# Optimization experiments

Measured on AMD Instinct MI355X. Metric: run time of the kernel, lower is better.

## Reference

```python
import jax, jax.numpy as jnp
import numpy as np

N = 100000      # nodes
E = 1600000     # edges
FX = 128        # raw node feature dim
MAXZ = 100      # z embedding / one-hot size
HID = 128       # hidden_channels
NL = 3          # num_layers
G = 512         # num graphs
BN_EPS = 1e-5


def _lin(key, din, dout):
    return jax.random.normal(key, (din, dout), jnp.float32) * (1.0 / np.sqrt(din))


def setup_inputs() -> dict:
    key = jax.random.key(0)
    ks = jax.random.split(key, 64)
    d = {}
    d["x"] = jax.random.normal(ks[0], (N, FX), jnp.float32)
    d["z"] = jax.random.randint(ks[1], (N,), 0, MAXZ)
    d["edge_index"] = jax.random.randint(ks[2], (2, E), 0, N)
    d["batch"] = jnp.sort(jax.random.randint(ks[3], (N,), 0, G))
    in0 = FX + 2 * MAXZ  # z_emb concatenated twice (faithful to source)
    ki = 4
    for l in range(NL):
        din = in0 if l == 0 else HID
        d[f"W1_{l}"] = _lin(ks[ki], din, HID); ki += 1
        d[f"b1_{l}"] = jnp.zeros((HID,), jnp.float32)
        d[f"W2_{l}"] = _lin(ks[ki], HID, HID); ki += 1
        d[f"b2_{l}"] = jnp.zeros((HID,), jnp.float32)
        d[f"g_{l}"] = jnp.ones((HID,), jnp.float32)
        d[f"be_{l}"] = jnp.zeros((HID,), jnp.float32)
    d["Wl1"] = _lin(ks[ki], NL * HID, HID); ki += 1
    d["bl1"] = jnp.zeros((HID,), jnp.float32)
    d["Wl2"] = _lin(ks[ki], HID, 1); ki += 1
    d["bl2"] = jnp.zeros((1,), jnp.float32)
    return d


def _gin_layer(h, src, dst, W1, b1, W2, b2, g, be):
    # GINConv with eps=0: nn(x + sum_{j->i} x_j)
    agg = jax.ops.segment_sum(h[src], dst, num_segments=N)  # [N, d]
    m = h + agg
    m = jax.nn.relu(m @ W1 + b1)
    m = jax.nn.relu(m @ W2 + b2)
    # training-mode BatchNorm1d over node axis (biased variance)
    mu = m.mean(0)
    var = jnp.mean((m - mu) ** 2, axis=0)
    return (m - mu) * jax.lax.rsqrt(var + BN_EPS) * g + be


def reference(x, z, edge_index, batch,
              W1_0, b1_0, W2_0, b2_0, g_0, be_0,
              W1_1, b1_1, W2_1, b2_1, g_1, be_1,
              W1_2, b1_2, W2_2, b2_2, g_2, be_2,
              Wl1, bl1, Wl2, bl2):
    src, dst = edge_index[0], edge_index[1]
    z_emb = jax.nn.one_hot(z, MAXZ, dtype=jnp.float32)  # [N, MAXZ]
    h = jnp.concatenate([z_emb, x], axis=1)
    h = jnp.concatenate([z_emb, h], axis=1)  # faithful double concat -> [N, FX+2*MAXZ]
    params = [(W1_0, b1_0, W2_0, b2_0, g_0, be_0),
              (W1_1, b1_1, W2_1, b2_1, g_1, be_1),
              (W1_2, b1_2, W2_2, b2_2, g_2, be_2)]
    xs = []
    for p in params:
        h = _gin_layer(h, src, dst, *p)
        xs.append(h)
    hcat = jnp.concatenate(xs, axis=1)  # jumping knowledge: [N, NL*HID]
    # global_mean_pool over graph ids
    counts = jax.ops.segment_sum(jnp.ones((N,), jnp.float32), batch, num_segments=G)
    pooled = jax.ops.segment_sum(hcat, batch, num_segments=G) / jnp.maximum(counts, 1.0)[:, None]
    out = jax.nn.relu(pooled @ Wl1 + bl1)
    # dropout is identity in eval / reference mode
    out = out @ Wl2 + bl2  # [G, 1]
    return out
```

## Files before the change

kernel.cpp:

```cpp
#include <hip/hip_runtime.h>
#include <hip/hip_bf16.h>

#define NN 100000
#define NROWS_PAD 100032
#define EE 1600000
#define GG 512
#define NPB 256
#define NB  ((NN + NPB - 1) / NPB)
#define PCHUNK 4096
#define PBLOCKS ((EE + PCHUNK - 1) / PCHUNK)
#define SBANK 8
static constexpr float BN_EPS = 1e-5f;

typedef _Float16 half8 __attribute__((ext_vector_type(8)));
typedef float floatx4 __attribute__((ext_vector_type(4)));


__global__ __launch_bounds__(256) void k_bhist(const int* __restrict__ EI,
                                               int* __restrict__ bcount)
{
    __shared__ int h[NB];
    const int t = threadIdx.x;
    for (int i = t; i < NB; i += 256) h[i] = 0;
    __syncthreads();
    const int e0 = blockIdx.x * PCHUNK;
    const int e1 = (e0 + PCHUNK < EE) ? e0 + PCHUNK : EE;
    for (int e = e0 + t; e < e1; e += 256)
        atomicAdd(&h[EI[EE + e] >> 8], 1);
    __syncthreads();
    for (int i = t; i < NB; i += 256)
        if (h[i]) atomicAdd(&bcount[i], h[i]);
}

__global__ __launch_bounds__(512) void k_bscan(const int* __restrict__ bcount,
                                               int* __restrict__ bstart,
                                               int* __restrict__ bcursor,
                                               int* __restrict__ row_start)
{
    __shared__ int s[512];
    int t = threadIdx.x;
    int v = (t < NB) ? bcount[t] : 0;
    s[t] = v;
    __syncthreads();
    for (int off = 1; off < 512; off <<= 1) {
        int u = (t >= off) ? s[t - off] : 0;
        __syncthreads();
        s[t] += u;
        __syncthreads();
    }
    if (t < NB) { int ex = s[t] - v; bstart[t] = ex; bcursor[t] = ex; }
    if (t == 0) { bstart[NB] = EE; row_start[NN] = EE; }
}

__global__ __launch_bounds__(256) void k_part(const int* __restrict__ EI,
                                              int* __restrict__ bcursor,
                                              int* __restrict__ ebuf)
{
    __shared__ int h[NB];
    __shared__ int cur[NB];
    const int t = threadIdx.x;
    for (int i = t; i < NB; i += 256) h[i] = 0;
    __syncthreads();
    const int e0 = blockIdx.x * PCHUNK;
    const int e1 = (e0 + PCHUNK < EE) ? e0 + PCHUNK : EE;
    for (int e = e0 + t; e < e1; e += 256)
        atomicAdd(&h[EI[EE + e] >> 8], 1);
    __syncthreads();
    for (int i = t; i < NB; i += 256)
        cur[i] = h[i] ? atomicAdd(&bcursor[i], h[i]) : 0;
    __syncthreads();
    for (int e = e0 + t; e < e1; e += 256) {
        int s = EI[e], d = EI[EE + e];
        int pos = atomicAdd(&cur[d >> 8], 1);
        ebuf[pos] = s | ((d & (NPB - 1)) << 17);
    }
}

__global__ __launch_bounds__(256) void k_csrbucket(const int* __restrict__ ebuf,
                                                   const int* __restrict__ bstart,
                                                   int* __restrict__ row_start,
                                                   int* __restrict__ ssrc)
{
    __shared__ int cnt[NPB];
    __shared__ int cur[NPB];
    const int b = blockIdx.x, t = threadIdx.x;
    cnt[t] = 0;
    __syncthreads();
    const int e0 = bstart[b], e1 = bstart[b + 1];
    for (int e = e0 + t; e < e1; e += 256) {
        unsigned p = (unsigned)__builtin_nontemporal_load(&ebuf[e]);
        atomicAdd(&cnt[p >> 17], 1);
    }
    __syncthreads();
    int myc = cnt[t];
    for (int off = 1; off < 256; off <<= 1) {
        int u = (t >= off) ? cnt[t - off] : 0;
        __syncthreads();
        cnt[t] += u;
        __syncthreads();
    }
    int pos0 = e0 + cnt[t] - myc;
    int idx = b * NPB + t;
    if (idx < NN) row_start[idx] = pos0;
    cur[t] = pos0;
    __syncthreads();
    for (int e = e0 + t; e < e1; e += 256) {
        unsigned p = (unsigned)__builtin_nontemporal_load(&ebuf[e]);
        int pos = atomicAdd(&cur[p >> 17], 1);
        ssrc[pos] = (int)(p & 0x1FFFFu);
    }
}


__global__ __launch_bounds__(256) void k_xcast(const float* __restrict__ X,
                                               _Float16* __restrict__ Xh)
{
    int idx = blockIdx.x * 256 + threadIdx.x;
    const float4* src = (const float4*)X;
    float4 a = src[idx * 2], b = src[idx * 2 + 1];
    half8 o = { (_Float16)a.x, (_Float16)a.y, (_Float16)a.z, (_Float16)a.w,
                (_Float16)b.x, (_Float16)b.y, (_Float16)b.z, (_Float16)b.w };
    *(half8*)&Xh[idx * 8] = o;
}

__device__ __forceinline__ void bn_sc_sh(const float* statsL,
                                         const float* g, const float* be, int k,
                                         float& sc, float& sh)
{
    float cs = 0.f, cq = 0.f;
    #pragma unroll
    for (int b = 0; b < SBANK; ++b) {
        cs += statsL[b * 256 + k];
        cq += statsL[b * 256 + 128 + k];
    }
    float inv_n = 1.0f / (float)NN;
    float mu = cs * inv_n;
    float var = cq * inv_n - mu * mu;
    sc = g[k] * rsqrtf(var + BN_EPS);
    sh = be[k] - mu * sc;
}

__global__ __launch_bounds__(256) void k_prep(
    const float* __restrict__ W1, const float* __restrict__ W2,
    const float* __restrict__ statsPrev,
    const float* __restrict__ g, const float* __restrict__ be,
    _Float16* __restrict__ Wt1, _Float16* __restrict__ Wt2,
    float* __restrict__ cvec, int l)
{
    int b = blockIdx.x, t = threadIdx.x;
    if (b < 64) {
        int idx = b * 256 + t;
        int n = idx >> 7, k = idx & 127;
        if (l == 0) {
            Wt1[idx] = (_Float16)W1[(200 + k) * 128 + n];
        } else {
            float sc, sh;
            bn_sc_sh(statsPrev, g, be, k, sc, sh);
            Wt1[idx] = (_Float16)(sc * W1[k * 128 + n]);
        }
    } else if (b < 128) {
        int idx = (b - 64) * 256 + t;
        int n = idx >> 7, k = idx & 127;
        Wt2[idx] = (_Float16)W2[k * 128 + n];
    } else if (t < 128) {
        float acc = 0.f;
        if (l != 0) {
            for (int k = 0; k < 128; ++k) {
                float sc, sh;
                bn_sc_sh(statsPrev, g, be, k, sc, sh);
                acc = fmaf(sh, W1[k * 128 + t], acc);
            }
        }
        cvec[t] = acc;
    }
}


#define MM_CORE_G(Ah, Wth)                                                   \
    const int lane = tid & 63;                                               \
    const int wv = tid >> 6;                                                 \
    const int ml = lane & 15;                                                \
    const int quad = lane >> 4;                                              \
    const int wr = wv >> 1, wc = wv & 1;                                     \
    floatx4 acc[2][4];                                                       \
    for (int r = 0; r < 2; ++r)                                              \
        for (int t = 0; t < 4; ++t)                                          \
            acc[r][t] = (floatx4){0.f, 0.f, 0.f, 0.f};                       \
    {                                                                        \
        const size_t ar0 = (size_t)(row0 + 32 * wr + ml) * 128;              \
        const size_t ar1 = ar0 + (size_t)16 * 128;                           \
        _Pragma("unroll")                                                    \
        for (int kq = 0; kq < 4; ++kq) {                                     \
            int k0 = kq * 32;                                                \
            half8 a0 = *(const half8*)&Ah[ar0 + k0 + quad * 8];              \
            half8 a1 = *(const half8*)&Ah[ar1 + k0 + quad * 8];              \
            _Pragma("unroll")                                                \
            for (int t = 0; t < 4; ++t) {                                    \
                half8 bf = *(const half8*)&Wth[(size_t)(64 * wc + 16 * t + ml) * 128 + k0 + quad * 8]; \
                acc[0][t] = __builtin_amdgcn_mfma_f32_16x16x32_f16(a0, bf, acc[0][t], 0, 0, 0); \
                acc[1][t] = __builtin_amdgcn_mfma_f32_16x16x32_f16(a1, bf, acc[1][t], 0, 0, 0); \
            }                                                                \
        }                                                                    \
    }

__global__ __launch_bounds__(256) void k_mm_embed(
    const _Float16* __restrict__ Ah, const _Float16* __restrict__ Wth,
    const int* __restrict__ Z, const float* __restrict__ W1,
    _Float16* __restrict__ Ph)
{
    const int tid = threadIdx.x;
    const int row0 = blockIdx.x * 64;
    MM_CORE_G(Ah, Wth)
    #pragma unroll
    for (int r = 0; r < 2; ++r)
        #pragma unroll
        for (int j = 0; j < 4; ++j) {
            int grow = row0 + 32 * wr + 16 * r + quad * 4 + j;
            if (grow < NN) {
                int zv = Z[grow];
                const float* w0 = &W1[zv * 128];
                const float* w1 = &W1[(100 + zv) * 128];
                #pragma unroll
                for (int t = 0; t < 4; ++t) {
                    int gcol = 64 * wc + 16 * t + ml;
                    float v = acc[r][t][j] + w0[gcol] + w1[gcol];
                    Ph[(size_t)grow * 128 + gcol] = (_Float16)v;
                }
            }
        }
}

__global__ __launch_bounds__(256) void k_mm1(
    const _Float16* __restrict__ Ah, const _Float16* __restrict__ Wth,
    _Float16* __restrict__ Ph)
{
    const int tid = threadIdx.x;
    const int row0 = blockIdx.x * 64;
    MM_CORE_G(Ah, Wth)
    #pragma unroll
    for (int r = 0; r < 2; ++r)
        #pragma unroll
        for (int j = 0; j < 4; ++j) {
            int grow = row0 + 32 * wr + 16 * r + quad * 4 + j;
            if (grow < NN) {
                #pragma unroll
                for (int t = 0; t < 4; ++t) {
                    int gcol = 64 * wc + 16 * t + ml;
                    Ph[(size_t)grow * 128 + gcol] = (_Float16)acc[r][t][j];
                }
            }
        }
}

__global__ __launch_bounds__(256) void k_mm2(
    const _Float16* __restrict__ Ah, const _Float16* __restrict__ Wth,
    const float* __restrict__ b2, _Float16* __restrict__ Oh,
    float* __restrict__ statsL)
{
    __shared__ float cs[128];
    __shared__ float cq[128];
    const int tid = threadIdx.x;
    const int row0 = blockIdx.x * 64;
    if (tid < 128) { cs[tid] = 0.f; cq[tid] = 0.f; }
    __syncthreads();

    MM_CORE_G(Ah, Wth)

    float b2v[4];
    #pragma unroll
    for (int t = 0; t < 4; ++t) b2v[t] = b2[64 * wc + 16 * t + ml];
    float st[4] = {0.f, 0.f, 0.f, 0.f};
    float qt[4] = {0.f, 0.f, 0.f, 0.f};
    #pragma unroll
    for (int r = 0; r < 2; ++r)
        #pragma unroll
        for (int j = 0; j < 4; ++j) {
            int grow = row0 + 32 * wr + 16 * r + quad * 4 + j;
            if (grow < NN) {
                #pragma unroll
                for (int t = 0; t < 4; ++t) {
                    int gcol = 64 * wc + 16 * t + ml;
                    float v = fmaxf(acc[r][t][j] + b2v[t], 0.f);
                    Oh[(size_t)grow * 128 + gcol] = (_Float16)v;
                    st[t] += v;
                    qt[t] += v * v;
                }
            }
        }
    #pragma unroll
    for (int t = 0; t < 4; ++t) {
        int gcol = 64 * wc + 16 * t + ml;
        atomicAdd(&cs[gcol], st[t]);
        atomicAdd(&cq[gcol], qt[t]);
    }
    __syncthreads();
    if (tid < 128) {
        float* bank = statsL + (blockIdx.x & (SBANK - 1)) * 256;
        atomicAdd(&bank[tid], cs[tid]);
        atomicAdd(&bank[128 + tid], cq[tid]);
    }
}


__global__ __launch_bounds__(256) void k_aggregate(
    const _Float16* __restrict__ Ph, const int* __restrict__ row_start,
    const int* __restrict__ ssrc, const float* __restrict__ b1,
    const float* __restrict__ cvec, _Float16* __restrict__ Mh)
{
    int idx = blockIdx.x * 256 + threadIdx.x;
    int node = idx >> 4, q = idx & 15;
    if (node >= NN) return;
    int s0 = row_start[node], s1 = row_start[node + 1];
    float degp1 = (float)(s1 - s0 + 1);
    float acc[8];
    half8 pv = *(const half8*)&Ph[(size_t)node * 128 + q * 8];
    #pragma unroll
    for (int j = 0; j < 8; ++j)
        acc[j] = (float)pv[j] + fmaf(degp1, cvec[q * 8 + j], b1[q * 8 + j]);
    int e = s0;
    for (; e + 7 < s1; e += 8) {
        int sidx[8];
        #pragma unroll
        for (int u = 0; u < 8; ++u)
            sidx[u] = __builtin_nontemporal_load(&ssrc[e + u]);
        half8 v[8];
        #pragma unroll
        for (int u = 0; u < 8; ++u)
            v[u] = *(const half8*)&Ph[(size_t)sidx[u] * 128 + q * 8];
        #pragma unroll
        for (int j = 0; j < 8; ++j)
            acc[j] += (((float)v[0][j] + (float)v[1][j]) + ((float)v[2][j] + (float)v[3][j]))
                    + (((float)v[4][j] + (float)v[5][j]) + ((float)v[6][j] + (float)v[7][j]));
    }
    for (; e + 1 < s1; e += 2) {
        int sa = __builtin_nontemporal_load(&ssrc[e]);
        int sb = __builtin_nontemporal_load(&ssrc[e + 1]);
        half8 va = *(const half8*)&Ph[(size_t)sa * 128 + q * 8];
        half8 vb = *(const half8*)&Ph[(size_t)sb * 128 + q * 8];
        #pragma unroll
        for (int j = 0; j < 8; ++j) acc[j] += (float)va[j] + (float)vb[j];
    }
    if (e < s1) {
        int sa = __builtin_nontemporal_load(&ssrc[e]);
        half8 va = *(const half8*)&Ph[(size_t)sa * 128 + q * 8];
        #pragma unroll
        for (int j = 0; j < 8; ++j) acc[j] += (float)va[j];
    }
    half8 o;
    #pragma unroll
    for (int j = 0; j < 8; ++j) o[j] = (_Float16)fmaxf(acc[j], 0.f);
    __builtin_nontemporal_store(o, (half8*)&Mh[(size_t)node * 128 + q * 8]);
}


__global__ __launch_bounds__(128) void k_pool(
    const _Float16* __restrict__ Ah, const int* __restrict__ batch,
    const float* __restrict__ statsL,
    const float* __restrict__ g_, const float* __restrict__ be,
    float* __restrict__ pooled, int loff)
{
    __shared__ float red[8][128];
    int g = blockIdx.x;
    int t = threadIdx.x;
    int rg = t >> 4, seg = t & 15;
    int lo = 0, hi = NN;
    while (lo < hi) { int mid = (lo + hi) >> 1; if (batch[mid] < g) lo = mid + 1; else hi = mid; }
    int s = lo;
    lo = s; hi = NN;
    while (lo < hi) { int mid = (lo + hi) >> 1; if (batch[mid] < g + 1) lo = mid + 1; else hi = mid; }
    int e = lo;
    float acc[8] = {};
    for (int i = s + rg; i < e; i += 8) {
        half8 v = *(const half8*)&Ah[(size_t)i * 128 + seg * 8];
        #pragma unroll
        for (int j = 0; j < 8; ++j) acc[j] += (float)v[j];
    }
    #pragma unroll
    for (int j = 0; j < 8; ++j) red[rg][seg * 8 + j] = acc[j];
    __syncthreads();
    int cnt = e - s;
    float inv = 1.0f / (float)(cnt > 0 ? cnt : 1);
    if (t < 128) {
        float s_ = 0.f;
        #pragma unroll
        for (int r = 0; r < 8; ++r) s_ += red[r][t];
        float sc, sh;
        bn_sc_sh(statsL, g_, be, t, sc, sh);
        pooled[g * 384 + loff + t] = fmaf(sc, s_ * inv, sh);
    }
}

__global__ __launch_bounds__(128) void k_final(
    const float* __restrict__ pooled,
    const float* __restrict__ Wl1, const float* __restrict__ bl1,
    const float* __restrict__ Wl2, const float* __restrict__ bl2,
    float* __restrict__ out)
{
    __shared__ float pr[384];
    __shared__ float red[128];
    int g = blockIdx.x, j = threadIdx.x;
    for (int i = j; i < 384; i += 128) pr[i] = pooled[g * 384 + i];
    __syncthreads();
    float acc = bl1[j];
    for (int k = 0; k < 384; ++k) acc = fmaf(pr[k], Wl1[k * 128 + j], acc);
    float r = fmaxf(acc, 0.f) * Wl2[j];
    red[j] = r;
    __syncthreads();
    for (int off = 64; off > 0; off >>= 1) {
        if (j < off) red[j] += red[j + off];
        __syncthreads();
    }
    if (j == 0) out[g] = red[0] + bl2[0];
}

extern "C" void kernel_launch(void* const* d_in, const int* in_sizes, int n_in,
                              void* d_out, int out_size, void* d_ws, size_t ws_size,
                              hipStream_t stream)
{
    const float* x     = (const float*)d_in[0];
    const int*   z     = (const int*)d_in[1];
    const int*   ei    = (const int*)d_in[2];
    const int*   batch = (const int*)d_in[3];
    const float* W1a[3] = {(const float*)d_in[4],  (const float*)d_in[10], (const float*)d_in[16]};
    const float* b1a[3] = {(const float*)d_in[5],  (const float*)d_in[11], (const float*)d_in[17]};
    const float* W2a[3] = {(const float*)d_in[6],  (const float*)d_in[12], (const float*)d_in[18]};
    const float* b2a[3] = {(const float*)d_in[7],  (const float*)d_in[13], (const float*)d_in[19]};
    const float* ga[3]  = {(const float*)d_in[8],  (const float*)d_in[14], (const float*)d_in[20]};
    const float* bea[3] = {(const float*)d_in[9],  (const float*)d_in[15], (const float*)d_in[21]};
    const float* Wl1 = (const float*)d_in[22];
    const float* bl1 = (const float*)d_in[23];
    const float* Wl2 = (const float*)d_in[24];
    const float* bl2 = (const float*)d_in[25];
    float* out = (float*)d_out;

    char* ws = (char*)d_ws;
    size_t off = 0;
    auto alloc = [&](size_t bytes) {
        void* p = ws + off;
        off += (bytes + 255) & ~(size_t)255;
        return p;
    };
    _Float16* Xh  = (_Float16*)alloc((size_t)NROWS_PAD * 128 * 2);
    _Float16* Ph  = (_Float16*)alloc((size_t)NROWS_PAD * 128 * 2);
    _Float16* Mh  = (_Float16*)alloc((size_t)NROWS_PAD * 128 * 2);
    _Float16* Ahb = (_Float16*)alloc((size_t)NROWS_PAD * 128 * 2);
    _Float16* Wt1 = (_Float16*)alloc((size_t)128 * 128 * 2);
    _Float16* Wt2 = (_Float16*)alloc((size_t)128 * 128 * 2);
    int*   ebuf     = (int*)alloc((size_t)EE * 4);
    int*   ssrc     = (int*)alloc((size_t)EE * 4);
    int*   row_st   = (int*)alloc((size_t)(NN + 1) * 4);
    int*   bcount   = (int*)alloc((size_t)NB * 4);
    int*   bstart   = (int*)alloc((size_t)(NB + 1) * 4);
    int*   bcursor  = (int*)alloc((size_t)NB * 4);
    float* cvec     = (float*)alloc(128 * 4);
    float* stats    = (float*)alloc((size_t)3 * SBANK * 256 * 4);
    float* pooled   = (float*)alloc((size_t)GG * 384 * 4);

    const int gemmBlocks = (NN + 63) / 64;
    const int aggBlocks  = (NN * 16 + 255) / 256;

    hipMemsetAsync(stats, 0, (size_t)3 * SBANK * 256 * 4, stream);
    hipMemsetAsync(bcount, 0, (size_t)NB * 4, stream);
    k_xcast<<<(NN * 128 / 8 + 255) / 256, 256, 0, stream>>>(x, Xh);
    k_bhist<<<PBLOCKS, 256, 0, stream>>>(ei, bcount);
    k_bscan<<<1, 512, 0, stream>>>(bcount, bstart, bcursor, row_st);
    k_part<<<PBLOCKS, 256, 0, stream>>>(ei, bcursor, ebuf);
    k_csrbucket<<<NB, 256, 0, stream>>>(ebuf, bstart, row_st, ssrc);

    for (int l = 0; l < 3; ++l) {
        float* statsL   = stats + (size_t)l * SBANK * 256;
        const float* statsPrev = (l > 0) ? stats + (size_t)(l - 1) * SBANK * 256 : stats;
        const float* pg   = (l > 0) ? ga[l - 1] : ga[0];
        const float* pbe  = (l > 0) ? bea[l - 1] : bea[0];
        k_prep<<<129, 256, 0, stream>>>(W1a[l], W2a[l], statsPrev, pg, pbe,
                                        Wt1, Wt2, cvec, l);
        if (l == 0)
            k_mm_embed<<<gemmBlocks, 256, 0, stream>>>(Xh, Wt1, z, W1a[0], Ph);
        else
            k_mm1<<<gemmBlocks, 256, 0, stream>>>(Ahb, Wt1, Ph);
        k_aggregate<<<aggBlocks, 256, 0, stream>>>(Ph, row_st, ssrc, b1a[l], cvec, Mh);
        k_mm2<<<gemmBlocks, 256, 0, stream>>>(Mh, Wt2, b2a[l], Ahb, statsL);
        k_pool<<<GG, 128, 0, stream>>>(Ahb, batch, statsL, ga[l], bea[l],
                                       pooled, l * 128);
    }
    k_final<<<GG, 128, 0, stream>>>(pooled, Wl1, bl1, Wl2, bl2, out);
}
```

Before: 699.8 us.

## Sort nodes by degree to balance aggregate kernel wavefront work

Adds a degree histogram, a scan and a fill pass that build a permutation of nodes ordered by descending in-degree. The aggregate kernel then processes nodes in that order, so each wavefront handles nodes of similar degree and loop divergence is reduced. The cost is three small extra kernel launches and an extra indirection per node, and neighbouring slots now touch scattered node rows, which loses locality on Ph and Mh accesses.

```diff
diff --git a/kernel.cpp b/kernel.cpp
--- a/kernel.cpp
+++ b/kernel.cpp
@@ -10,6 +10,7 @@
 #define PCHUNK 4096
 #define PBLOCKS ((EE + PCHUNK - 1) / PCHUNK)
 #define SBANK 8
+#define DBIN 64
 static constexpr float BN_EPS = 1e-5f;
 
 typedef _Float16 half8 __attribute__((ext_vector_type(8)));
@@ -108,6 +109,46 @@
         unsigned p = (unsigned)__builtin_nontemporal_load(&ebuf[e]);
         int pos = atomicAdd(&cur[p >> 17], 1);
         ssrc[pos] = (int)(p & 0x1FFFFu);
+    }
+}
+
+
+__global__ __launch_bounds__(256) void k_dhist(const int* __restrict__ row_start,
+                                               int* __restrict__ dcount)
+{
+    __shared__ int h[DBIN];
+    const int t = threadIdx.x;
+    if (t < DBIN) h[t] = 0;
+    __syncthreads();
+    int i = blockIdx.x * 256 + t;
+    if (i < NN) {
+        int deg = row_start[i + 1] - row_start[i];
+        int bin = deg < DBIN ? deg : DBIN - 1;
+        atomicAdd(&h[bin], 1);
+    }
+    __syncthreads();
+    if (t < DBIN && h[t]) atomicAdd(&dcount[t], h[t]);
+}
+
+__global__ __launch_bounds__(64) void k_dscan(const int* __restrict__ dcount,
+                                              int* __restrict__ dcur)
+{
+    int b = threadIdx.x;
+    int off = 0;
+    for (int b2 = b + 1; b2 < DBIN; ++b2) off += dcount[b2];
+    dcur[b] = off;
+}
+
+__global__ __launch_bounds__(256) void k_dfill(const int* __restrict__ row_start,
+                                               int* __restrict__ dcur,
+                                               int* __restrict__ perm)
+{
+    int i = blockIdx.x * 256 + threadIdx.x;
+    if (i < NN) {
+        int deg = row_start[i + 1] - row_start[i];
+        int bin = deg < DBIN ? deg : DBIN - 1;
+        int pos = atomicAdd(&dcur[bin], 1);
+        perm[pos] = i;
     }
 }
 
@@ -304,12 +345,14 @@
 
 __global__ __launch_bounds__(256) void k_aggregate(
     const _Float16* __restrict__ Ph, const int* __restrict__ row_start,
-    const int* __restrict__ ssrc, const float* __restrict__ b1,
-    const float* __restrict__ cvec, _Float16* __restrict__ Mh)
+    const int* __restrict__ ssrc, const int* __restrict__ perm,
+    const float* __restrict__ b1, const float* __restrict__ cvec,
+    _Float16* __restrict__ Mh)
 {
     int idx = blockIdx.x * 256 + threadIdx.x;
-    int node = idx >> 4, q = idx & 15;
-    if (node >= NN) return;
+    int slot = idx >> 4, q = idx & 15;
+    if (slot >= NN) return;
+    int node = perm[slot];
     int s0 = row_start[node], s1 = row_start[node + 1];
     float degp1 = (float)(s1 - s0 + 1);
     float acc[8];
@@ -449,23 +492,31 @@
     int*   ebuf     = (int*)alloc((size_t)EE * 4);
     int*   ssrc     = (int*)alloc((size_t)EE * 4);
     int*   row_st   = (int*)alloc((size_t)(NN + 1) * 4);
+    int*   perm     = (int*)alloc((size_t)NN * 4);
     int*   bcount   = (int*)alloc((size_t)NB * 4);
     int*   bstart   = (int*)alloc((size_t)(NB + 1) * 4);
     int*   bcursor  = (int*)alloc((size_t)NB * 4);
+    int*   dcount   = (int*)alloc((size_t)DBIN * 4);
+    int*   dcur     = (int*)alloc((size_t)DBIN * 4);
     float* cvec     = (float*)alloc(128 * 4);
     float* stats    = (float*)alloc((size_t)3 * SBANK * 256 * 4);
     float* pooled   = (float*)alloc((size_t)GG * 384 * 4);
 
     const int gemmBlocks = (NN + 63) / 64;
     const int aggBlocks  = (NN * 16 + 255) / 256;
+    const int nodeBlocks = (NN + 255) / 256;
 
     hipMemsetAsync(stats, 0, (size_t)3 * SBANK * 256 * 4, stream);
     hipMemsetAsync(bcount, 0, (size_t)NB * 4, stream);
+    hipMemsetAsync(dcount, 0, (size_t)DBIN * 4, stream);
     k_xcast<<<(NN * 128 / 8 + 255) / 256, 256, 0, stream>>>(x, Xh);
     k_bhist<<<PBLOCKS, 256, 0, stream>>>(ei, bcount);
     k_bscan<<<1, 512, 0, stream>>>(bcount, bstart, bcursor, row_st);
     k_part<<<PBLOCKS, 256, 0, stream>>>(ei, bcursor, ebuf);
     k_csrbucket<<<NB, 256, 0, stream>>>(ebuf, bstart, row_st, ssrc);
+    k_dhist<<<nodeBlocks, 256, 0, stream>>>(row_st, dcount);
+    k_dscan<<<1, 64, 0, stream>>>(dcount, dcur);
+    k_dfill<<<nodeBlocks, 256, 0, stream>>>(row_st, dcur, perm);
 
     for (int l = 0; l < 3; ++l) {
         float* statsL   = stats + (size_t)l * SBANK * 256;
@@ -478,7 +529,8 @@
             k_mm_embed<<<gemmBlocks, 256, 0, stream>>>(Xh, Wt1, z, W1a[0], Ph);
         else
             k_mm1<<<gemmBlocks, 256, 0, stream>>>(Ahb, Wt1, Ph);
-        k_aggregate<<<aggBlocks, 256, 0, stream>>>(Ph, row_st, ssrc, b1a[l], cvec, Mh);
+        k_aggregate<<<aggBlocks, 256, 0, stream>>>(Ph, row_st, ssrc, perm,
+                                                   b1a[l], cvec, Mh);
         k_mm2<<<gemmBlocks, 256, 0, stream>>>(Mh, Wt2, b2a[l], Ahb, statsL);
         k_pool<<<GG, 128, 0, stream>>>(Ahb, batch, statsL, ga[l], bea[l],
                                        pooled, l * 128);
```

Result: slower. 978.6 us (+39.8%).

## Move BatchNorm statistics from GEMM epilogue atomics into per-graph pool reduction

Applied to the files above, without the earlier changes.

The per-column sum and sum-of-squares for BatchNorm are no longer accumulated with shared and global atomics in the mm2 epilogue. Instead, the pool kernel, which already reads every row, also accumulates squares and writes per-graph sums. A new single-block kernel reduces these over graphs into scale and shift vectors, and the final kernel applies the affine transform to the pooled means. This takes the atomics and extra syncs out of the GEMM and removes a memset, at the cost of an extra serial single-block launch per layer that loops over 512 graphs.

```diff
diff --git a/kernel.cpp b/kernel.cpp
--- a/kernel.cpp
+++ b/kernel.cpp
@@ -9,7 +9,6 @@
 #define NB  ((NN + NPB - 1) / NPB)
 #define PCHUNK 4096
 #define PBLOCKS ((EE + PCHUNK - 1) / PCHUNK)
-#define SBANK 8
 static constexpr float BN_EPS = 1e-5f;
 
 typedef _Float16 half8 __attribute__((ext_vector_type(8)));
@@ -123,27 +122,9 @@
     *(half8*)&Xh[idx * 8] = o;
 }
 
-__device__ __forceinline__ void bn_sc_sh(const float* statsL,
-                                         const float* g, const float* be, int k,
-                                         float& sc, float& sh)
-{
-    float cs = 0.f, cq = 0.f;
-    #pragma unroll
-    for (int b = 0; b < SBANK; ++b) {
-        cs += statsL[b * 256 + k];
-        cq += statsL[b * 256 + 128 + k];
-    }
-    float inv_n = 1.0f / (float)NN;
-    float mu = cs * inv_n;
-    float var = cq * inv_n - mu * mu;
-    sc = g[k] * rsqrtf(var + BN_EPS);
-    sh = be[k] - mu * sc;
-}
-
 __global__ __launch_bounds__(256) void k_prep(
     const float* __restrict__ W1, const float* __restrict__ W2,
-    const float* __restrict__ statsPrev,
-    const float* __restrict__ g, const float* __restrict__ be,
+    const float* __restrict__ scshPrev,
     _Float16* __restrict__ Wt1, _Float16* __restrict__ Wt2,
     float* __restrict__ cvec, int l)
 {
@@ -154,9 +135,7 @@
         if (l == 0) {
             Wt1[idx] = (_Float16)W1[(200 + k) * 128 + n];
         } else {
-            float sc, sh;
-            bn_sc_sh(statsPrev, g, be, k, sc, sh);
-            Wt1[idx] = (_Float16)(sc * W1[k * 128 + n]);
+            Wt1[idx] = (_Float16)(scshPrev[k] * W1[k * 128 + n]);
         }
     } else if (b < 128) {
         int idx = (b - 64) * 256 + t;
@@ -164,13 +143,9 @@
         Wt2[idx] = (_Float16)W2[k * 128 + n];
     } else if (t < 128) {
         float acc = 0.f;
-        if (l != 0) {
-            for (int k = 0; k < 128; ++k) {
-                float sc, sh;
-                bn_sc_sh(statsPrev, g, be, k, sc, sh);
-                acc = fmaf(sh, W1[k * 128 + t], acc);
-            }
-        }
+        if (l != 0)
+            for (int k = 0; k < 128; ++k)
+                acc = fmaf(scshPrev[128 + k], W1[k * 128 + t], acc);
         cvec[t] = acc;
     }
 }
@@ -254,23 +229,14 @@
 
 __global__ __launch_bounds__(256) void k_mm2(
     const _Float16* __restrict__ Ah, const _Float16* __restrict__ Wth,
-    const float* __restrict__ b2, _Float16* __restrict__ Oh,
-    float* __restrict__ statsL)
-{
-    __shared__ float cs[128];
-    __shared__ float cq[128];
+    const float* __restrict__ b2, _Float16* __restrict__ Oh)
+{
     const int tid = threadIdx.x;
     const int row0 = blockIdx.x * 64;
-    if (tid < 128) { cs[tid] = 0.f; cq[tid] = 0.f; }
-    __syncthreads();
-
     MM_CORE_G(Ah, Wth)
-
     float b2v[4];
     #pragma unroll
     for (int t = 0; t < 4; ++t) b2v[t] = b2[64 * wc + 16 * t + ml];
-    float st[4] = {0.f, 0.f, 0.f, 0.f};
-    float qt[4] = {0.f, 0.f, 0.f, 0.f};
     #pragma unroll
     for (int r = 0; r < 2; ++r)
         #pragma unroll
@@ -282,23 +248,9 @@
                     int gcol = 64 * wc + 16 * t + ml;
                     float v = fmaxf(acc[r][t][j] + b2v[t], 0.f);
                     Oh[(size_t)grow * 128 + gcol] = (_Float16)v;
-                    st[t] += v;
-                    qt[t] += v * v;
                 }
             }
         }
-    #pragma unroll
-    for (int t = 0; t < 4; ++t) {
-        int gcol = 64 * wc + 16 * t + ml;
-        atomicAdd(&cs[gcol], st[t]);
-        atomicAdd(&cq[gcol], qt[t]);
-    }
-    __syncthreads();
-    if (tid < 128) {
-        float* bank = statsL + (blockIdx.x & (SBANK - 1)) * 256;
-        atomicAdd(&bank[tid], cs[tid]);
-        atomicAdd(&bank[128 + tid], cq[tid]);
-    }
 }
 
 
@@ -355,9 +307,7 @@
 
 __global__ __launch_bounds__(128) void k_pool(
     const _Float16* __restrict__ Ah, const int* __restrict__ batch,
-    const float* __restrict__ statsL,
-    const float* __restrict__ g_, const float* __restrict__ be,
-    float* __restrict__ pooled, int loff)
+    float* __restrict__ gsum, float* __restrict__ gsq, int* __restrict__ gcnt)
 {
     __shared__ float red[8][128];
     int g = blockIdx.x;
@@ -370,28 +320,57 @@
     while (lo < hi) { int mid = (lo + hi) >> 1; if (batch[mid] < g + 1) lo = mid + 1; else hi = mid; }
     int e = lo;
     float acc[8] = {};
+    float accq[8] = {};
     for (int i = s + rg; i < e; i += 8) {
         half8 v = *(const half8*)&Ah[(size_t)i * 128 + seg * 8];
         #pragma unroll
-        for (int j = 0; j < 8; ++j) acc[j] += (float)v[j];
+        for (int j = 0; j < 8; ++j) {
+            float f = (float)v[j];
+            acc[j] += f;
+            accq[j] += f * f;
+        }
     }
     #pragma unroll
     for (int j = 0; j < 8; ++j) red[rg][seg * 8 + j] = acc[j];
     __syncthreads();
-    int cnt = e - s;
-    float inv = 1.0f / (float)(cnt > 0 ? cnt : 1);
+    float s_ = 0.f;
+    #pragma unroll
+    for (int r = 0; r < 8; ++r) s_ += red[r][t];
+    __syncthreads();
+    #pragma unroll
+    for (int j = 0; j < 8; ++j) red[rg][seg * 8 + j] = accq[j];
+    __syncthreads();
+    float q_ = 0.f;
+    #pragma unroll
+    for (int r = 0; r < 8; ++r) q_ += red[r][t];
+    gsum[(size_t)g * 128 + t] = s_;
+    gsq[(size_t)g * 128 + t] = q_;
+    if (t == 0) gcnt[g] = (e - s) > 0 ? (e - s) : 1;
+}
+
+__global__ __launch_bounds__(256) void k_statsred(
+    const float* __restrict__ gsum, const float* __restrict__ gsq,
+    const float* __restrict__ g_, const float* __restrict__ be,
+    float* __restrict__ scsh)
+{
+    int t = threadIdx.x;
     if (t < 128) {
-        float s_ = 0.f;
-        #pragma unroll
-        for (int r = 0; r < 8; ++r) s_ += red[r][t];
-        float sc, sh;
-        bn_sc_sh(statsL, g_, be, t, sc, sh);
-        pooled[g * 384 + loff + t] = fmaf(sc, s_ * inv, sh);
+        float cs = 0.f;
+        for (int g = 0; g < GG; ++g) cs += gsum[(size_t)g * 128 + t];
+        float cq = 0.f;
+        for (int g = 0; g < GG; ++g) cq += gsq[(size_t)g * 128 + t];
+        float inv_n = 1.0f / (float)NN;
+        float mu = cs * inv_n;
+        float var = cq * inv_n - mu * mu;
+        float sc = g_[t] * rsqrtf(var + BN_EPS);
+        scsh[t] = sc;
+        scsh[128 + t] = be[t] - mu * sc;
     }
 }
 
 __global__ __launch_bounds__(128) void k_final(
-    const float* __restrict__ pooled,
+    const float* __restrict__ gsum, const int* __restrict__ gcnt,
+    const float* __restrict__ scsh,
     const float* __restrict__ Wl1, const float* __restrict__ bl1,
     const float* __restrict__ Wl2, const float* __restrict__ bl2,
     float* __restrict__ out)
@@ -399,7 +378,14 @@
     __shared__ float pr[384];
     __shared__ float red[128];
     int g = blockIdx.x, j = threadIdx.x;
-    for (int i = j; i < 384; i += 128) pr[i] = pooled[g * 384 + i];
+    float inv = 1.0f / (float)gcnt[g];
+    #pragma unroll
+    for (int l = 0; l < 3; ++l) {
+        float sc = scsh[l * 256 + j];
+        float sh = scsh[l * 256 + 128 + j];
+        float gs = gsum[((size_t)l * GG + g) * 128 + j];
+        pr[l * 128 + j] = fmaf(sc, gs * inv, sh);
+    }
     __syncthreads();
     float acc = bl1[j];
     for (int k = 0; k < 384; ++k) acc = fmaf(pr[k], Wl1[k * 128 + j], acc);
@@ -453,13 +439,16 @@
     int*   bstart   = (int*)alloc((size_t)(NB + 1) * 4);
     int*   bcursor  = (int*)alloc((size_t)NB * 4);
     float* cvec     = (float*)alloc(128 * 4);
-    float* stats    = (float*)alloc((size_t)3 * SBANK * 256 * 4);
+    float* gsum     = (float*)alloc((size_t)3 * GG * 128 * 4);
+    float* gsq      = (float*)alloc((size_t)GG * 128 * 4);
+    int*   gcnt     = (int*)alloc((size_t)GG * 4);
+    float* scsh     = (float*)alloc((size_t)3 * 256 * 4);
     float* pooled   = (float*)alloc((size_t)GG * 384 * 4);
+    (void)pooled;
 
     const int gemmBlocks = (NN + 63) / 64;
     const int aggBlocks  = (NN * 16 + 255) / 256;
 
-    hipMemsetAsync(stats, 0, (size_t)3 * SBANK * 256 * 4, stream);
     hipMemsetAsync(bcount, 0, (size_t)NB * 4, stream);
     k_xcast<<<(NN * 128 / 8 + 255) / 256, 256, 0, stream>>>(x, Xh);
     k_bhist<<<PBLOCKS, 256, 0, stream>>>(ei, bcount);
@@ -468,20 +457,18 @@
     k_csrbucket<<<NB, 256, 0, stream>>>(ebuf, bstart, row_st, ssrc);
 
     for (int l = 0; l < 3; ++l) {
-        float* statsL   = stats + (size_t)l * SBANK * 256;
-        const float* statsPrev = (l > 0) ? stats + (size_t)(l - 1) * SBANK * 256 : stats;
-        const float* pg   = (l > 0) ? ga[l - 1] : ga[0];
-        const float* pbe  = (l > 0) ? bea[l - 1] : bea[0];
-        k_prep<<<129, 256, 0, stream>>>(W1a[l], W2a[l], statsPrev, pg, pbe,
-                                        Wt1, Wt2, cvec, l);
+        float* gsumL = gsum + (size_t)l * GG * 128;
+        const float* scshPrev = (l > 0) ? scsh + (size_t)(l - 1) * 256 : scsh;
+        k_prep<<<129, 256, 0, stream>>>(W1a[l], W2a[l], scshPrev, Wt1, Wt2, cvec, l);
         if (l == 0)
             k_mm_embed<<<gemmBlocks, 256, 0, stream>>>(Xh, Wt1, z, W1a[0], Ph);
         else
             k_mm1<<<gemmBlocks, 256, 0, stream>>>(Ahb, Wt1, Ph);
         k_aggregate<<<aggBlocks, 256, 0, stream>>>(Ph, row_st, ssrc, b1a[l], cvec, Mh);
-        k_mm2<<<gemmBlocks, 256, 0, stream>>>(Mh, Wt2, b2a[l], Ahb, statsL);
-        k_pool<<<GG, 128, 0, stream>>>(Ahb, batch, statsL, ga[l], bea[l],
-                                       pooled, l * 128);
-    }
-    k_final<<<GG, 128, 0, stream>>>(pooled, Wl1, bl1, Wl2, bl2, out);
-}
+        k_mm2<<<gemmBlocks, 256, 0, stream>>>(Mh, Wt2, b2a[l], Ahb);
+        k_pool<<<GG, 128, 0, stream>>>(Ahb, batch, gsumL, gsq, gcnt);
+        k_statsred<<<1, 256, 0, stream>>>(gsumL, gsq, ga[l], bea[l],
+                                          scsh + (size_t)l * 256);
+    }
+    k_final<<<GG, 128, 0, stream>>>(gsum, gcnt, scsh, Wl1, bl1, Wl2, bl2, out);
+}
```

Measured after the change: 712.6 us. Within noise of the previous version (+1.8%).
